# Optimization experiments

Measured on AMD Instinct MI355X. Metric: run time of the kernel, lower is better.

The kernel has to match this reference:

```python
import jax, jax.numpy as jnp
import numpy as np

N_NODES = 100000
N_EDGES = 1000000
D_IN, D_HID, D_OUT = 20, 64, 64
NEG_SLOPE = 0.2


def _gat_layer(x, src, dst, W, a_src, a_dst, b, n_nodes):
    """PyG-style single-head GATConv: message j->i, softmax over incoming edges of i."""
    h = x @ W                                  # [N, D]
    alpha_s = h @ a_src                        # [N]
    alpha_d = h @ a_dst                        # [N]
    e = jax.nn.leaky_relu(alpha_s[src] + alpha_d[dst], NEG_SLOPE)  # [E]
    # numerically-stable segment softmax over destination nodes
    m = jax.ops.segment_max(e, dst, num_segments=n_nodes)          # [N]
    ex = jnp.exp(e - m[dst])                                       # [E]
    denom = jax.ops.segment_sum(ex, dst, num_segments=n_nodes)     # [N]
    alpha = ex / denom[dst]                                        # [E]
    out = jax.ops.segment_sum(alpha[:, None] * h[src], dst, num_segments=n_nodes)
    return out + b


def setup_inputs() -> dict:
    key = jax.random.key(0)
    ks = jax.random.split(key, 11)
    x = jax.random.normal(ks[0], (N_NODES, D_IN), dtype=jnp.float32)
    edge_index = jax.random.randint(ks[1], (2, N_EDGES), 0, N_NODES, dtype=jnp.int64)
    s1 = 1.0 / np.sqrt(D_IN)
    s2 = 1.0 / np.sqrt(D_HID)
    return {
        "x": x,
        "edge_index": edge_index,
        "W1": jax.random.normal(ks[2], (D_IN, D_HID), dtype=jnp.float32) * s1,
        "a_src1": jax.random.normal(ks[3], (D_HID,), dtype=jnp.float32) * s2,
        "a_dst1": jax.random.normal(ks[4], (D_HID,), dtype=jnp.float32) * s2,
        "b1": jnp.zeros((D_HID,), dtype=jnp.float32),
        "W2": jax.random.normal(ks[5], (D_HID, D_OUT), dtype=jnp.float32) * s2,
        "a_src2": jax.random.normal(ks[6], (D_OUT,), dtype=jnp.float32) * s2,
        "a_dst2": jax.random.normal(ks[7], (D_OUT,), dtype=jnp.float32) * s2,
        "b2": jnp.zeros((D_OUT,), dtype=jnp.float32),
    }


def reference(x, edge_index, W1, a_src1, a_dst1, b1, W2, a_src2, a_dst2, b2):
    n = x.shape[0]
    # PyG GATConv adds self-loops by default
    loops = jnp.arange(n, dtype=edge_index.dtype)
    src = jnp.concatenate([edge_index[0], loops])
    dst = jnp.concatenate([edge_index[1], loops])
    h = _gat_layer(x, src, dst, W1, a_src1, a_dst1, b1, n)
    h = jax.nn.relu(h)
    # dropout(p=0.2) is identity in eval mode
    h = _gat_layer(h, src, dst, W2, a_src2, a_dst2, b2, n)
    # global_mean_pool with all-zero batch -> mean over all nodes, shape [1, D_OUT]
    return jnp.mean(h, axis=0, keepdims=True)
```

## Files before the change

### kernel.cpp

```cpp
#include <hip/hip_runtime.h>
#include <math.h>

#define NDIM 64
#define LRELU_SLOPE 0.2f
#define BSHIFT 8
#define BNODES 256
#define ECAP 3584
#define CCAP (ECAP + BNODES)

typedef float f32x2 __attribute__((ext_vector_type(2)));

__device__ __forceinline__ ushort f2bf(float f) {
    unsigned u = __float_as_uint(f);
    unsigned r = (u + 0x7fffu + ((u >> 16) & 1u)) >> 16;
    return (ushort)r;
}
__device__ __forceinline__ float bflo(unsigned u) { return __uint_as_float(u << 16); }
__device__ __forceinline__ float bfhi(unsigned u) { return __uint_as_float(u & 0xffff0000u); }

__global__ __launch_bounds__(256) void pg_kernel(
    const int* __restrict__ src, const int* __restrict__ dst,
    int* __restrict__ bcur, unsigned* __restrict__ part, int E, int nb, int PB,
    const float* __restrict__ X, const float* __restrict__ W,
    const float* __restrict__ asrc, const float* __restrict__ adst,
    unsigned char* __restrict__ h, float* __restrict__ as_,
    float* __restrict__ ad_, int N) {
    int t = threadIdx.x;
    if ((int)blockIdx.x < PB) {
        __shared__ int hist[512];
        __shared__ int base[512];
        for (int i = t; i < nb; i += 256) hist[i] = 0;
        __syncthreads();
        int chunk = blockIdx.x * 2048;
        int s[8], d[8];
#pragma unroll
        for (int j = 0; j < 2; ++j) {
            int idx = chunk + j * 1024 + t * 4;
            if (idx + 3 < E) {
                int4 sv = *(const int4*)(src + idx);
                int4 dv = *(const int4*)(dst + idx);
                s[j*4+0]=sv.x; s[j*4+1]=sv.y; s[j*4+2]=sv.z; s[j*4+3]=sv.w;
                d[j*4+0]=dv.x; d[j*4+1]=dv.y; d[j*4+2]=dv.z; d[j*4+3]=dv.w;
            } else {
#pragma unroll
                for (int q = 0; q < 4; ++q) {
                    int i2 = idx + q;
                    if (i2 < E) { s[j*4+q] = src[i2]; d[j*4+q] = dst[i2]; }
                    else        { s[j*4+q] = 0;       d[j*4+q] = -1; }
                }
            }
        }
#pragma unroll
        for (int j = 0; j < 8; ++j)
            if (d[j] >= 0) atomicAdd(&hist[d[j] >> BSHIFT], 1);
        __syncthreads();
        for (int i = t; i < nb; i += 256) {
            int c = hist[i];
            base[i] = c ? atomicAdd(&bcur[i], c) : 0;
            hist[i] = 0;
        }
        __syncthreads();
#pragma unroll
        for (int j = 0; j < 8; ++j) {
            if (d[j] >= 0) {
                int b = d[j] >> BSHIFT;
                int loc = base[b] + atomicAdd(&hist[b], 1);
                if (loc > ECAP - 1) loc = ECAP - 1;
                part[(size_t)b * ECAP + loc] =
                    ((unsigned)(d[j] & (BNODES - 1)) << 17) | (unsigned)s[j];
            }
        }
    } else {
        const int K = 20, KS = 32;
        __shared__ float xs[64 * 32];
        __shared__ unsigned hsq[64 * 17];
        __shared__ float ps[2][4][64];
        int base2 = (blockIdx.x - PB) * 64;
        for (int i = t; i < 64 * KS; i += 256) {
            int nl = i / KS, k = i - nl * KS;
            int node = base2 + nl;
            float v = (k < K && node < N) ? X[(size_t)node * K + k] : 0.f;
            xs[nl * KS + ((k + nl) & (KS - 1))] = v;
        }
        __syncthreads();
        int wid = __builtin_amdgcn_readfirstlane(t >> 6);
        int lane = t & 63;
        int node = base2 + lane;
        float acc[16];
#pragma unroll
        for (int j = 0; j < 16; ++j) acc[j] = 0.f;
        const float* Wg = W + wid * 16;
        const float* xrow = xs + lane * KS;
#pragma unroll 4
        for (int k = 0; k < K; ++k) {
            float xk = xrow[(k + lane) & (KS - 1)];
#pragma unroll
            for (int j = 0; j < 16; ++j)
                acc[j] = fmaf(xk, Wg[k * 64 + j], acc[j]);
        }
        float s = 0.f, d = 0.f;
#pragma unroll
        for (int j = 0; j < 16; ++j) {
            s = fmaf(acc[j], asrc[wid * 16 + j], s);
            d = fmaf(acc[j], adst[wid * 16 + j], d);
        }
        ps[0][wid][lane] = s;
        ps[1][wid][lane] = d;
#pragma unroll
        for (int j = 0; j < 16; j += 4) {
            int q = (wid * 16 + j) >> 2;
            int sp = (q + lane) & 15;
            int u = __builtin_amdgcn_cvt_pk_fp8_f32(acc[j], acc[j + 1], 0, false);
            u = __builtin_amdgcn_cvt_pk_fp8_f32(acc[j + 2], acc[j + 3], u, true);
            hsq[lane * 17 + sp] = (unsigned)u;
        }
        __syncthreads();
        if (wid == 0) {
            float s4 = ps[0][0][lane] + ps[0][1][lane] + ps[0][2][lane] + ps[0][3][lane];
            float d4 = ps[1][0][lane] + ps[1][1][lane] + ps[1][2][lane] + ps[1][3][lane];
            if (node < N) { as_[node] = s4; ad_[node] = d4; }
        }
        unsigned* hout = (unsigned*)h;
        for (int pass = 0; pass < 4; ++pass) {
            int row = pass * 16 + (t >> 4);
            int q = t & 15;
            int sp = (q + row) & 15;
            unsigned v = hsq[row * 17 + sp];
            int n2 = base2 + row;
            if (n2 < N) hout[(size_t)n2 * 16 + q] = v;
        }
    }
}

__global__ __launch_bounds__(256) void csr_kernel(
    const int* __restrict__ bcur, const unsigned* __restrict__ part,
    int* __restrict__ csr, int2* __restrict__ offlen, int N,
    const float* __restrict__ W2, const float* __restrict__ a_src2,
    const float* __restrict__ a_dst2, float* __restrict__ atil) {
    __shared__ int hist[256];
    __shared__ int sc[256];
    int b = blockIdx.x, t = threadIdx.x;
    int nodeBase = b << BSHIFT;
    int nNodes = min(BNODES, N - nodeBase);
    int count = min(bcur[b], ECAP);
    hist[t] = (t < nNodes) ? 1 : 0;
    __syncthreads();
    const unsigned* slice = part + (size_t)b * ECAP;
    for (int i = t; i < count; i += 256) {
        int dl = (int)(slice[i] >> 17);
        atomicAdd(&hist[dl], 1);
    }
    __syncthreads();
    int cnt = hist[t];
    sc[t] = cnt;
    __syncthreads();
    for (int o = 1; o < 256; o <<= 1) {
        int v = sc[t];
        int u = (t >= o) ? sc[t - o] : 0;
        __syncthreads();
        sc[t] = v + u;
        __syncthreads();
    }
    int excl = sc[t] - cnt;
    int boff = b * CCAP;
    if (t < nNodes) {
        offlen[nodeBase + t] = make_int2(boff + excl, cnt);
        csr[boff + excl] = nodeBase + t;
    }
    hist[t] = excl + 1;
    __syncthreads();
    for (int i = t; i < count; i += 256) {
        unsigned e = slice[i];
        int dl = (int)(e >> 17);
        int pos = boff + atomicAdd(&hist[dl], 1);
        csr[pos] = (int)(e & 0x1ffffu);
    }
    if (b == 0 && t < 128) {
        int j = t & 63;
        const float* av = (t < 64) ? a_src2 : a_dst2;
        const float* wr = W2 + (size_t)j * 64;
        float s = 0.f;
#pragma unroll 8
        for (int k = 0; k < 64; ++k) s = fmaf(wr[k], av[k], s);
        atil[t] = s;
    }
}

__global__ __launch_bounds__(256) void agg1_kernel(
    const int2* __restrict__ offlen, const int* __restrict__ csr,
    const float* __restrict__ as_, const float* __restrict__ ad_,
    const unsigned char* __restrict__ hsrc, const float* __restrict__ bias,
    const float* __restrict__ atil,
    ushort* __restrict__ out, float* __restrict__ as2,
    float* __restrict__ ad2, int n) {
    int wid = threadIdx.x >> 6, lane = threadIdx.x & 63;
    int half = lane >> 5;
    int lh = lane & 31;
    int g = lh >> 3;
    int l = lane & 7;
    int hw = wid * 2 + half;
    int node = blockIdx.x * 8 + hw;
    int base_lane = lane & 32;
    if (node < n) {
        int2 ol = offlen[node];
        int off = ol.x, len = ol.y;
        float adi = ad_[node];
        bool vpre = lh < len;
        int skpre = vpre ? csr[off + lh] : 0;
        float apre = vpre ? as_[skpre] : 0.f;
        float tpre = apre + adi;
        tpre = (tpre > 0.f) ? tpre : LRELU_SLOPE * tpre;
        float expre = vpre ? __expf(tpre) : 0.f;
        float den = expre;
        den += __shfl_xor(den, 1);
        den += __shfl_xor(den, 2);
        den += __shfl_xor(den, 4);
        den += __shfl_xor(den, 8);
        den += __shfl_xor(den, 16);
        float acc[8];
#pragma unroll
        for (int j = 0; j < 8; ++j) acc[j] = 0.f;
        if (__all(len <= 32)) {
            uint2 hv[8];
            float exs[8];
#pragma unroll
            for (int c = 0; c < 8; ++c) {
                int e = c * 4 + g;
                int sk = __shfl(skpre, base_lane + e);
                exs[c] = __shfl(expre, base_lane + e);
                const uint2* p = (const uint2*)(hsrc + ((size_t)sk << 6) + (l << 3));
                hv[c] = (e < len) ? *p : make_uint2(0u, 0u);
            }
#pragma unroll
            for (int c = 0; c < 8; ++c) {
                float ex = exs[c];
                f32x2 p0 = __builtin_amdgcn_cvt_pk_f32_fp8(hv[c].x, false);
                f32x2 p1 = __builtin_amdgcn_cvt_pk_f32_fp8(hv[c].x, true);
                f32x2 p2 = __builtin_amdgcn_cvt_pk_f32_fp8(hv[c].y, false);
                f32x2 p3 = __builtin_amdgcn_cvt_pk_f32_fp8(hv[c].y, true);
                acc[0] = fmaf(ex, p0.x, acc[0]);
                acc[1] = fmaf(ex, p0.y, acc[1]);
                acc[2] = fmaf(ex, p1.x, acc[2]);
                acc[3] = fmaf(ex, p1.y, acc[3]);
                acc[4] = fmaf(ex, p2.x, acc[4]);
                acc[5] = fmaf(ex, p2.y, acc[5]);
                acc[6] = fmaf(ex, p3.x, acc[6]);
                acc[7] = fmaf(ex, p3.y, acc[7]);
            }
        } else {
            float den_tail = 0.f;
            int niter = (len + 3) >> 2;
            int sk0 = __shfl(skpre, base_lane + g);
            float ex0 = __shfl(expre, base_lane + g);
            bool ve0 = g < len;
            uint2 hv0 = make_uint2(0, 0);
            if (ve0) hv0 = *(const uint2*)(hsrc + ((size_t)sk0 << 6) + (l << 3));
            int sk1 = __shfl(skpre, base_lane + 4 + g);
            float ex1 = __shfl(expre, base_lane + 4 + g);
            bool ve1 = (4 + g) < len;
            uint2 hv1 = make_uint2(0, 0);
            if (ve1) hv1 = *(const uint2*)(hsrc + ((size_t)sk1 << 6) + (l << 3));
            for (int i = 0; i < niter; ++i) {
                float ex = ex0;
                uint2 hv = hv0;
                ex0 = ex1; hv0 = hv1;
                int e2 = (i + 2) * 4 + g;
                bool ve2 = e2 < len;
                int esrc = e2 < 32 ? e2 : 31;
                sk1 = __shfl(skpre, base_lane + esrc);
                ex1 = __shfl(expre, base_lane + esrc);
                if (e2 >= 32) {
                    if (ve2) {
                        sk1 = csr[off + e2];
                        float a = as_[sk1];
                        float tt = a + adi;
                        tt = (tt > 0.f) ? tt : LRELU_SLOPE * tt;
                        ex1 = __expf(tt);
                        den_tail += ex1;
                    } else ex1 = 0.f;
                }
                hv1 = make_uint2(0, 0);
                if (ve2) hv1 = *(const uint2*)(hsrc + ((size_t)sk1 << 6) + (l << 3));
                f32x2 p0 = __builtin_amdgcn_cvt_pk_f32_fp8(hv.x, false);
                f32x2 p1 = __builtin_amdgcn_cvt_pk_f32_fp8(hv.x, true);
                f32x2 p2 = __builtin_amdgcn_cvt_pk_f32_fp8(hv.y, false);
                f32x2 p3 = __builtin_amdgcn_cvt_pk_f32_fp8(hv.y, true);
                acc[0] = fmaf(ex, p0.x, acc[0]);
                acc[1] = fmaf(ex, p0.y, acc[1]);
                acc[2] = fmaf(ex, p1.x, acc[2]);
                acc[3] = fmaf(ex, p1.y, acc[3]);
                acc[4] = fmaf(ex, p2.x, acc[4]);
                acc[5] = fmaf(ex, p2.y, acc[5]);
                acc[6] = fmaf(ex, p3.x, acc[6]);
                acc[7] = fmaf(ex, p3.y, acc[7]);
            }
            den_tail += __shfl_xor(den_tail, 8);
            den_tail += __shfl_xor(den_tail, 16);
            den += den_tail;
        }
#pragma unroll
        for (int j = 0; j < 8; ++j) {
            acc[j] += __shfl_xor(acc[j], 8);
            acc[j] += __shfl_xor(acc[j], 16);
        }
        float inv = 1.f / den;
        const float4 bv0 = *(const float4*)(bias + l * 8);
        const float4 bv1 = *(const float4*)(bias + l * 8 + 4);
        float v[8];
        v[0] = fmaxf(fmaf(acc[0], inv, bv0.x), 0.f);
        v[1] = fmaxf(fmaf(acc[1], inv, bv0.y), 0.f);
        v[2] = fmaxf(fmaf(acc[2], inv, bv0.z), 0.f);
        v[3] = fmaxf(fmaf(acc[3], inv, bv0.w), 0.f);
        v[4] = fmaxf(fmaf(acc[4], inv, bv1.x), 0.f);
        v[5] = fmaxf(fmaf(acc[5], inv, bv1.y), 0.f);
        v[6] = fmaxf(fmaf(acc[6], inv, bv1.z), 0.f);
        v[7] = fmaxf(fmaf(acc[7], inv, bv1.w), 0.f);
        if (g == 0) {
            uint4 pk;
            pk.x = (unsigned)f2bf(v[0]) | ((unsigned)f2bf(v[1]) << 16);
            pk.y = (unsigned)f2bf(v[2]) | ((unsigned)f2bf(v[3]) << 16);
            pk.z = (unsigned)f2bf(v[4]) | ((unsigned)f2bf(v[5]) << 16);
            pk.w = (unsigned)f2bf(v[6]) | ((unsigned)f2bf(v[7]) << 16);
            *(uint4*)(out + (size_t)node * NDIM + l * 8) = pk;
        }
        const float4 s0 = *(const float4*)(atil + l * 8);
        const float4 s1 = *(const float4*)(atil + l * 8 + 4);
        const float4 d0 = *(const float4*)(atil + 64 + l * 8);
        const float4 d1 = *(const float4*)(atil + 64 + l * 8 + 4);
        float sp = v[0]*s0.x + v[1]*s0.y + v[2]*s0.z + v[3]*s0.w
                 + v[4]*s1.x + v[5]*s1.y + v[6]*s1.z + v[7]*s1.w;
        float dp = v[0]*d0.x + v[1]*d0.y + v[2]*d0.z + v[3]*d0.w
                 + v[4]*d1.x + v[5]*d1.y + v[6]*d1.z + v[7]*d1.w;
        sp += __shfl_xor(sp, 1); sp += __shfl_xor(sp, 2); sp += __shfl_xor(sp, 4);
        dp += __shfl_xor(dp, 1); dp += __shfl_xor(dp, 2); dp += __shfl_xor(dp, 4);
        if (lh == 0) { as2[node] = sp; ad2[node] = dp; }
    }
}

__global__ __launch_bounds__(256) void agg2_kernel(
    const int2* __restrict__ offlen, const int* __restrict__ csr,
    const float* __restrict__ as_, const float* __restrict__ ad_,
    const ushort* __restrict__ osrc, float* __restrict__ pool, int n) {
    __shared__ float psum[8][NDIM];
    int wid = threadIdx.x >> 6, lane = threadIdx.x & 63;
    int half = lane >> 5;
    int lh = lane & 31;
    int g = lh >> 3;
    int l = lane & 7;
    int hw = wid * 2 + half;
    int node = blockIdx.x * 8 + hw;
    int base_lane = lane & 32;
    float v[8];
#pragma unroll
    for (int j = 0; j < 8; ++j) v[j] = 0.f;
    if (node < n) {
        int2 ol = offlen[node];
        int off = ol.x, len = ol.y;
        float adi = ad_[node];
        bool vpre = lh < len;
        int skpre = vpre ? csr[off + lh] : 0;
        float apre = vpre ? as_[skpre] : 0.f;
        float tpre = apre + adi;
        tpre = (tpre > 0.f) ? tpre : LRELU_SLOPE * tpre;
        float expre = vpre ? __expf(tpre) : 0.f;
        float den = expre;
        den += __shfl_xor(den, 1);
        den += __shfl_xor(den, 2);
        den += __shfl_xor(den, 4);
        den += __shfl_xor(den, 8);
        den += __shfl_xor(den, 16);
        float acc[8];
#pragma unroll
        for (int j = 0; j < 8; ++j) acc[j] = 0.f;
        if (__all(len <= 32)) {
            uint4 hv[8];
            float exs[8];
#pragma unroll
            for (int c = 0; c < 8; ++c) {
                int e = c * 4 + g;
                int sk = __shfl(skpre, base_lane + e);
                exs[c] = __shfl(expre, base_lane + e);
                const uint4* p = (const uint4*)(osrc + ((size_t)sk << 6) + (l << 3));
                hv[c] = (e < len) ? *p : make_uint4(0u, 0u, 0u, 0u);
            }
#pragma unroll
            for (int c = 0; c < 8; ++c) {
                float ex = exs[c];
                acc[0] = fmaf(ex, bflo(hv[c].x), acc[0]);
                acc[1] = fmaf(ex, bfhi(hv[c].x), acc[1]);
                acc[2] = fmaf(ex, bflo(hv[c].y), acc[2]);
                acc[3] = fmaf(ex, bfhi(hv[c].y), acc[3]);
                acc[4] = fmaf(ex, bflo(hv[c].z), acc[4]);
                acc[5] = fmaf(ex, bfhi(hv[c].z), acc[5]);
                acc[6] = fmaf(ex, bflo(hv[c].w), acc[6]);
                acc[7] = fmaf(ex, bfhi(hv[c].w), acc[7]);
            }
        } else {
            float den_tail = 0.f;
            int niter = (len + 3) >> 2;
            int sk0 = __shfl(skpre, base_lane + g);
            float ex0 = __shfl(expre, base_lane + g);
            bool ve0 = g < len;
            uint4 hv0 = make_uint4(0, 0, 0, 0);
            if (ve0) hv0 = *(const uint4*)(osrc + ((size_t)sk0 << 6) + (l << 3));
            int sk1 = __shfl(skpre, base_lane + 4 + g);
            float ex1 = __shfl(expre, base_lane + 4 + g);
            bool ve1 = (4 + g) < len;
            uint4 hv1 = make_uint4(0, 0, 0, 0);
            if (ve1) hv1 = *(const uint4*)(osrc + ((size_t)sk1 << 6) + (l << 3));
            for (int i = 0; i < niter; ++i) {
                float ex = ex0;
                uint4 hv = hv0;
                ex0 = ex1; hv0 = hv1;
                int e2 = (i + 2) * 4 + g;
                bool ve2 = e2 < len;
                int esrc = e2 < 32 ? e2 : 31;
                sk1 = __shfl(skpre, base_lane + esrc);
                ex1 = __shfl(expre, base_lane + esrc);
                if (e2 >= 32) {
                    if (ve2) {
                        sk1 = csr[off + e2];
                        float a = as_[sk1];
                        float tt = a + adi;
                        tt = (tt > 0.f) ? tt : LRELU_SLOPE * tt;
                        ex1 = __expf(tt);
                        den_tail += ex1;
                    } else ex1 = 0.f;
                }
                hv1 = make_uint4(0, 0, 0, 0);
                if (ve2) hv1 = *(const uint4*)(osrc + ((size_t)sk1 << 6) + (l << 3));
                acc[0] = fmaf(ex, bflo(hv.x), acc[0]);
                acc[1] = fmaf(ex, bfhi(hv.x), acc[1]);
                acc[2] = fmaf(ex, bflo(hv.y), acc[2]);
                acc[3] = fmaf(ex, bfhi(hv.y), acc[3]);
                acc[4] = fmaf(ex, bflo(hv.z), acc[4]);
                acc[5] = fmaf(ex, bfhi(hv.z), acc[5]);
                acc[6] = fmaf(ex, bflo(hv.w), acc[6]);
                acc[7] = fmaf(ex, bfhi(hv.w), acc[7]);
            }
            den_tail += __shfl_xor(den_tail, 8);
            den_tail += __shfl_xor(den_tail, 16);
            den += den_tail;
        }
#pragma unroll
        for (int j = 0; j < 8; ++j) {
            acc[j] += __shfl_xor(acc[j], 8);
            acc[j] += __shfl_xor(acc[j], 16);
        }
        float inv = 1.f / den;
#pragma unroll
        for (int j = 0; j < 8; ++j) v[j] = acc[j] * inv;
    }
    if (g == 0) {
#pragma unroll
        for (int j = 0; j < 8; ++j) psum[hw][l * 8 + j] = v[j];
    }
    __syncthreads();
    if (threadIdx.x < NDIM) {
        float t = 0.f;
#pragma unroll
        for (int r = 0; r < 8; ++r) t += psum[r][threadIdx.x];
        pool[(size_t)blockIdx.x * NDIM + threadIdx.x] = t;
    }
}

__global__ void mean_kernel(const float* __restrict__ pool,
                            const float* __restrict__ W2,
                            const float* __restrict__ b2,
                            float* __restrict__ out, int nb, float invn) {
    __shared__ float sm[4][NDIM];
    __shared__ float zs[NDIM];
    int lane = threadIdx.x & 63, wid = threadIdx.x >> 6;
    int row = blockIdx.x * 4 + wid;
    int stride = gridDim.x * 4;
    float s = 0.f;
    for (int i = row; i < nb; i += stride) s += pool[(long)i * NDIM + lane];
    sm[wid][lane] = s;
    __syncthreads();
    if (wid == 0) {
        zs[lane] = sm[0][lane] + sm[1][lane] + sm[2][lane] + sm[3][lane];
    }
    __syncthreads();
    if (wid == 0) {
        float y = 0.f;
#pragma unroll 8
        for (int j = 0; j < 64; ++j)
            y = fmaf(zs[j], W2[(size_t)j * 64 + lane], y);
        atomicAdd(&out[lane], y * invn);
        if (blockIdx.x == 0) atomicAdd(&out[lane], b2[lane]);
    }
}

extern "C" void kernel_launch(void* const* d_in, const int* in_sizes, int n_in,
                              void* d_out, int out_size, void* d_ws, size_t ws_size,
                              hipStream_t stream) {
    const float* x      = (const float*)d_in[0];
    const int*   eidx   = (const int*)d_in[1];
    const float* W1     = (const float*)d_in[2];
    const float* a_src1 = (const float*)d_in[3];
    const float* a_dst1 = (const float*)d_in[4];
    const float* b1     = (const float*)d_in[5];
    const float* W2     = (const float*)d_in[6];
    const float* a_src2 = (const float*)d_in[7];
    const float* a_dst2 = (const float*)d_in[8];
    const float* b2     = (const float*)d_in[9];
    float* out = (float*)d_out;

    const int N = in_sizes[0] / 20;
    const int E = in_sizes[1] / 2;
    const int* src = eidx;
    const int* dst = eidx + E;
    const int NB = (N + BNODES - 1) >> BSHIFT;

    const int gemm_blocks = (N + 63) / 64;
    const int agg_blocks  = (N + 7) / 8;
    const int PB = (E + 2047) / 2048;

    char* ws = (char*)d_ws;
    unsigned char* h = (unsigned char*)ws;
    ushort* o   = (ushort*)(h + (size_t)N * NDIM);
    float* as1  = (float*)(o + (size_t)N * NDIM);
    float* ad1  = as1 + N;
    float* as2  = ad1 + N;
    float* ad2  = as2 + N;
    int2*  offlen = (int2*)(ad2 + N);
    int*   csr  = (int*)(offlen + N);
    float* pool = (float*)(csr + (size_t)NB * CCAP);
    float* atil = pool + (size_t)agg_blocks * NDIM;
    int*   bcur = (int*)(atil + 128);
    unsigned* part = (unsigned*)(bcur + NB);

    hipMemsetAsync(d_out, 0, (size_t)out_size * sizeof(float), stream);
    hipMemsetAsync(bcur, 0, (size_t)NB * sizeof(int), stream);

    pg_kernel<<<PB + gemm_blocks, 256, 0, stream>>>(
        src, dst, bcur, part, E, NB, PB,
        x, W1, a_src1, a_dst1, h, as1, ad1, N);
    csr_kernel<<<NB, 256, 0, stream>>>(bcur, part, csr, offlen, N,
                                       W2, a_src2, a_dst2, atil);

    agg1_kernel<<<agg_blocks, 256, 0, stream>>>(
        offlen, csr, as1, ad1, h, b1, atil, o, as2, ad2, N);

    agg2_kernel<<<agg_blocks, 256, 0, stream>>>(
        offlen, csr, as2, ad2, o, pool, N);

    mean_kernel<<<64, 256, 0, stream>>>(pool, W2, b2, out, agg_blocks,
                                        1.0f / (float)N);
}
```

Before: 193.8 us.

## Store layer-1 output as FP8 and share a packed-math gather helper

The layer-1 aggregated activations are now stored as FP8 instead of bf16, which halves the bytes gathered per edge in the second aggregation kernel. Both aggregation kernels now call a common gather routine that accumulates with packed two-wide f32 multiply-adds and skips chunks that are fully past the longest row in the wave pair. Out-of-range nodes are clamped rather than branched around. The cost is lower precision in the intermediate activations, which may move the result further from the reference.

```diff
diff --git a/kernel.cpp b/kernel.cpp
--- a/kernel.cpp
+++ b/kernel.cpp
@@ -10,11 +10,6 @@
 
 typedef float f32x2 __attribute__((ext_vector_type(2)));
 
-__device__ __forceinline__ ushort f2bf(float f) {
-    unsigned u = __float_as_uint(f);
-    unsigned r = (u + 0x7fffu + ((u >> 16) & 1u)) >> 16;
-    return (ushort)r;
-}
 __device__ __forceinline__ float bflo(unsigned u) { return __uint_as_float(u << 16); }
 __device__ __forceinline__ float bfhi(unsigned u) { return __uint_as_float(u & 0xffff0000u); }
 
@@ -186,12 +181,110 @@
     }
 }
 
+__device__ __forceinline__ float gather64(
+    int off, int len, int lm, float adi, int lh, int g, int l, int base_lane,
+    const int* __restrict__ csr, const float* __restrict__ as_,
+    const unsigned char* __restrict__ rows, float acc[8]) {
+    bool vpre = lh < len;
+    int skpre = vpre ? csr[off + lh] : 0;
+    float apre = vpre ? as_[skpre] : 0.f;
+    float tpre = apre + adi;
+    tpre = (tpre > 0.f) ? tpre : LRELU_SLOPE * tpre;
+    float expre = vpre ? __expf(tpre) : 0.f;
+    float den = expre;
+    den += __shfl_xor(den, 1);
+    den += __shfl_xor(den, 2);
+    den += __shfl_xor(den, 4);
+    den += __shfl_xor(den, 8);
+    den += __shfl_xor(den, 16);
+    f32x2 a01 = {0.f, 0.f}, a23 = {0.f, 0.f}, a45 = {0.f, 0.f}, a67 = {0.f, 0.f};
+    if (__all(lm <= 32)) {
+        uint2 hv[8];
+        float exs[8];
+#pragma unroll
+        for (int c = 0; c < 8; ++c) {
+            hv[c] = make_uint2(0u, 0u);
+            exs[c] = 0.f;
+            if (c * 4 < lm) {
+                int e = c * 4 + g;
+                int sk = __shfl(skpre, base_lane + e);
+                exs[c] = __shfl(expre, base_lane + e);
+                if (e < len)
+                    hv[c] = *(const uint2*)(rows + ((size_t)sk << 6) + (l << 3));
+            }
+        }
+#pragma unroll
+        for (int c = 0; c < 8; ++c) {
+            if (c * 4 < len) {
+                f32x2 ex2 = {exs[c], exs[c]};
+                a01 += __builtin_amdgcn_cvt_pk_f32_fp8(hv[c].x, false) * ex2;
+                a23 += __builtin_amdgcn_cvt_pk_f32_fp8(hv[c].x, true) * ex2;
+                a45 += __builtin_amdgcn_cvt_pk_f32_fp8(hv[c].y, false) * ex2;
+                a67 += __builtin_amdgcn_cvt_pk_f32_fp8(hv[c].y, true) * ex2;
+            }
+        }
+    } else {
+        float den_tail = 0.f;
+        int niter = (len + 3) >> 2;
+        int sk0 = __shfl(skpre, base_lane + g);
+        float ex0 = __shfl(expre, base_lane + g);
+        bool ve0 = g < len;
+        uint2 hv0 = make_uint2(0, 0);
+        if (ve0) hv0 = *(const uint2*)(rows + ((size_t)sk0 << 6) + (l << 3));
+        int sk1 = __shfl(skpre, base_lane + 4 + g);
+        float ex1 = __shfl(expre, base_lane + 4 + g);
+        bool ve1 = (4 + g) < len;
+        uint2 hv1 = make_uint2(0, 0);
+        if (ve1) hv1 = *(const uint2*)(rows + ((size_t)sk1 << 6) + (l << 3));
+        for (int i = 0; i < niter; ++i) {
+            float ex = ex0;
+            uint2 hv = hv0;
+            ex0 = ex1; hv0 = hv1;
+            int e2 = (i + 2) * 4 + g;
+            bool ve2 = e2 < len;
+            int esrc = e2 < 32 ? e2 : 31;
+            sk1 = __shfl(skpre, base_lane + esrc);
+            ex1 = __shfl(expre, base_lane + esrc);
+            if (e2 >= 32) {
+                if (ve2) {
+                    sk1 = csr[off + e2];
+                    float a = as_[sk1];
+                    float tt = a + adi;
+                    tt = (tt > 0.f) ? tt : LRELU_SLOPE * tt;
+                    ex1 = __expf(tt);
+                    den_tail += ex1;
+                } else ex1 = 0.f;
+            }
+            hv1 = make_uint2(0, 0);
+            if (ve2) hv1 = *(const uint2*)(rows + ((size_t)sk1 << 6) + (l << 3));
+            f32x2 ex2 = {ex, ex};
+            a01 += __builtin_amdgcn_cvt_pk_f32_fp8(hv.x, false) * ex2;
+            a23 += __builtin_amdgcn_cvt_pk_f32_fp8(hv.x, true) * ex2;
+            a45 += __builtin_amdgcn_cvt_pk_f32_fp8(hv.y, false) * ex2;
+            a67 += __builtin_amdgcn_cvt_pk_f32_fp8(hv.y, true) * ex2;
+        }
+        den_tail += __shfl_xor(den_tail, 8);
+        den_tail += __shfl_xor(den_tail, 16);
+        den += den_tail;
+    }
+    acc[0] = a01.x; acc[1] = a01.y;
+    acc[2] = a23.x; acc[3] = a23.y;
+    acc[4] = a45.x; acc[5] = a45.y;
+    acc[6] = a67.x; acc[7] = a67.y;
+#pragma unroll
+    for (int j = 0; j < 8; ++j) {
+        acc[j] += __shfl_xor(acc[j], 8);
+        acc[j] += __shfl_xor(acc[j], 16);
+    }
+    return den;
+}
+
 __global__ __launch_bounds__(256) void agg1_kernel(
     const int2* __restrict__ offlen, const int* __restrict__ csr,
     const float* __restrict__ as_, const float* __restrict__ ad_,
     const unsigned char* __restrict__ hsrc, const float* __restrict__ bias,
     const float* __restrict__ atil,
-    ushort* __restrict__ out, float* __restrict__ as2,
+    unsigned char* __restrict__ o8, float* __restrict__ as2,
     float* __restrict__ ad2, int n) {
     int wid = threadIdx.x >> 6, lane = threadIdx.x & 63;
     int half = lane >> 5;
@@ -201,108 +294,16 @@
     int hw = wid * 2 + half;
     int node = blockIdx.x * 8 + hw;
     int base_lane = lane & 32;
+    int nodec = min(node, n - 1);
+    int2 ol = offlen[nodec];
+    int off = ol.x;
+    int len = (node < n) ? ol.y : 0;
+    float adi = ad_[nodec];
+    int lm = max(len, __shfl_xor(len, 32));
+    float acc[8];
+    float den = gather64(off, len, lm, adi, lh, g, l, base_lane,
+                         csr, as_, hsrc, acc);
     if (node < n) {
-        int2 ol = offlen[node];
-        int off = ol.x, len = ol.y;
-        float adi = ad_[node];
-        bool vpre = lh < len;
-        int skpre = vpre ? csr[off + lh] : 0;
-        float apre = vpre ? as_[skpre] : 0.f;
-        float tpre = apre + adi;
-        tpre = (tpre > 0.f) ? tpre : LRELU_SLOPE * tpre;
-        float expre = vpre ? __expf(tpre) : 0.f;
-        float den = expre;
-        den += __shfl_xor(den, 1);
-        den += __shfl_xor(den, 2);
-        den += __shfl_xor(den, 4);
-        den += __shfl_xor(den, 8);
-        den += __shfl_xor(den, 16);
-        float acc[8];
-#pragma unroll
-        for (int j = 0; j < 8; ++j) acc[j] = 0.f;
-        if (__all(len <= 32)) {
-            uint2 hv[8];
-            float exs[8];
-#pragma unroll
-            for (int c = 0; c < 8; ++c) {
-                int e = c * 4 + g;
-                int sk = __shfl(skpre, base_lane + e);
-                exs[c] = __shfl(expre, base_lane + e);
-                const uint2* p = (const uint2*)(hsrc + ((size_t)sk << 6) + (l << 3));
-                hv[c] = (e < len) ? *p : make_uint2(0u, 0u);
-            }
-#pragma unroll
-            for (int c = 0; c < 8; ++c) {
-                float ex = exs[c];
-                f32x2 p0 = __builtin_amdgcn_cvt_pk_f32_fp8(hv[c].x, false);
-                f32x2 p1 = __builtin_amdgcn_cvt_pk_f32_fp8(hv[c].x, true);
-                f32x2 p2 = __builtin_amdgcn_cvt_pk_f32_fp8(hv[c].y, false);
-                f32x2 p3 = __builtin_amdgcn_cvt_pk_f32_fp8(hv[c].y, true);
-                acc[0] = fmaf(ex, p0.x, acc[0]);
-                acc[1] = fmaf(ex, p0.y, acc[1]);
-                acc[2] = fmaf(ex, p1.x, acc[2]);
-                acc[3] = fmaf(ex, p1.y, acc[3]);
-                acc[4] = fmaf(ex, p2.x, acc[4]);
-                acc[5] = fmaf(ex, p2.y, acc[5]);
-                acc[6] = fmaf(ex, p3.x, acc[6]);
-                acc[7] = fmaf(ex, p3.y, acc[7]);
-            }
-        } else {
-            float den_tail = 0.f;
-            int niter = (len + 3) >> 2;
-            int sk0 = __shfl(skpre, base_lane + g);
-            float ex0 = __shfl(expre, base_lane + g);
-            bool ve0 = g < len;
-            uint2 hv0 = make_uint2(0, 0);
-            if (ve0) hv0 = *(const uint2*)(hsrc + ((size_t)sk0 << 6) + (l << 3));
-            int sk1 = __shfl(skpre, base_lane + 4 + g);
-            float ex1 = __shfl(expre, base_lane + 4 + g);
-            bool ve1 = (4 + g) < len;
-            uint2 hv1 = make_uint2(0, 0);
-            if (ve1) hv1 = *(const uint2*)(hsrc + ((size_t)sk1 << 6) + (l << 3));
-            for (int i = 0; i < niter; ++i) {
-                float ex = ex0;
-                uint2 hv = hv0;
-                ex0 = ex1; hv0 = hv1;
-                int e2 = (i + 2) * 4 + g;
-                bool ve2 = e2 < len;
-                int esrc = e2 < 32 ? e2 : 31;
-                sk1 = __shfl(skpre, base_lane + esrc);
-                ex1 = __shfl(expre, base_lane + esrc);
-                if (e2 >= 32) {
-                    if (ve2) {
-                        sk1 = csr[off + e2];
-                        float a = as_[sk1];
-                        float tt = a + adi;
-                        tt = (tt > 0.f) ? tt : LRELU_SLOPE * tt;
-                        ex1 = __expf(tt);
-                        den_tail += ex1;
-                    } else ex1 = 0.f;
-                }
-                hv1 = make_uint2(0, 0);
-                if (ve2) hv1 = *(const uint2*)(hsrc + ((size_t)sk1 << 6) + (l << 3));
-                f32x2 p0 = __builtin_amdgcn_cvt_pk_f32_fp8(hv.x, false);
-                f32x2 p1 = __builtin_amdgcn_cvt_pk_f32_fp8(hv.x, true);
-                f32x2 p2 = __builtin_amdgcn_cvt_pk_f32_fp8(hv.y, false);
-                f32x2 p3 = __builtin_amdgcn_cvt_pk_f32_fp8(hv.y, true);
-                acc[0] = fmaf(ex, p0.x, acc[0]);
-                acc[1] = fmaf(ex, p0.y, acc[1]);
-                acc[2] = fmaf(ex, p1.x, acc[2]);
-                acc[3] = fmaf(ex, p1.y, acc[3]);
-                acc[4] = fmaf(ex, p2.x, acc[4]);
-                acc[5] = fmaf(ex, p2.y, acc[5]);
-                acc[6] = fmaf(ex, p3.x, acc[6]);
-                acc[7] = fmaf(ex, p3.y, acc[7]);
-            }
-            den_tail += __shfl_xor(den_tail, 8);
-            den_tail += __shfl_xor(den_tail, 16);
-            den += den_tail;
-        }
-#pragma unroll
-        for (int j = 0; j < 8; ++j) {
-            acc[j] += __shfl_xor(acc[j], 8);
-            acc[j] += __shfl_xor(acc[j], 16);
-        }
         float inv = 1.f / den;
         const float4 bv0 = *(const float4*)(bias + l * 8);
         const float4 bv1 = *(const float4*)(bias + l * 8 + 4);
@@ -316,12 +317,12 @@
         v[6] = fmaxf(fmaf(acc[6], inv, bv1.z), 0.f);
         v[7] = fmaxf(fmaf(acc[7], inv, bv1.w), 0.f);
         if (g == 0) {
-            uint4 pk;
-            pk.x = (unsigned)f2bf(v[0]) | ((unsigned)f2bf(v[1]) << 16);
-            pk.y = (unsigned)f2bf(v[2]) | ((unsigned)f2bf(v[3]) << 16);
-            pk.z = (unsigned)f2bf(v[4]) | ((unsigned)f2bf(v[5]) << 16);
-            pk.w = (unsigned)f2bf(v[6]) | ((unsigned)f2bf(v[7]) << 16);
-            *(uint4*)(out + (size_t)node * NDIM + l * 8) = pk;
+            int u0 = __builtin_amdgcn_cvt_pk_fp8_f32(v[0], v[1], 0, false);
+            u0 = __builtin_amdgcn_cvt_pk_fp8_f32(v[2], v[3], u0, true);
+            int u1 = __builtin_amdgcn_cvt_pk_fp8_f32(v[4], v[5], 0, false);
+            u1 = __builtin_amdgcn_cvt_pk_fp8_f32(v[6], v[7], u1, true);
+            *(uint2*)(o8 + ((size_t)node << 6) + (l << 3)) =
+                make_uint2((unsigned)u0, (unsigned)u1);
         }
         const float4 s0 = *(const float4*)(atil + l * 8);
         const float4 s1 = *(const float4*)(atil + l * 8 + 4);
@@ -340,7 +341,7 @@
 __global__ __launch_bounds__(256) void agg2_kernel(
     const int2* __restrict__ offlen, const int* __restrict__ csr,
     const float* __restrict__ as_, const float* __restrict__ ad_,
-    const ushort* __restrict__ osrc, float* __restrict__ pool, int n) {
+    const unsigned char* __restrict__ osrc, float* __restrict__ pool, int n) {
     __shared__ float psum[8][NDIM];
     int wid = threadIdx.x >> 6, lane = threadIdx.x & 63;
     int half = lane >> 5;
@@ -350,103 +351,19 @@
     int hw = wid * 2 + half;
     int node = blockIdx.x * 8 + hw;
     int base_lane = lane & 32;
+    int nodec = min(node, n - 1);
+    int2 ol = offlen[nodec];
+    int off = ol.x;
+    int len = (node < n) ? ol.y : 0;
+    float adi = ad_[nodec];
+    int lm = max(len, __shfl_xor(len, 32));
+    float acc[8];
+    float den = gather64(off, len, lm, adi, lh, g, l, base_lane,
+                         csr, as_, osrc, acc);
     float v[8];
 #pragma unroll
     for (int j = 0; j < 8; ++j) v[j] = 0.f;
     if (node < n) {
-        int2 ol = offlen[node];
-        int off = ol.x, len = ol.y;
-        float adi = ad_[node];
-        bool vpre = lh < len;
-        int skpre = vpre ? csr[off + lh] : 0;
-        float apre = vpre ? as_[skpre] : 0.f;
-        float tpre = apre + adi;
-        tpre = (tpre > 0.f) ? tpre : LRELU_SLOPE * tpre;
-        float expre = vpre ? __expf(tpre) : 0.f;
-        float den = expre;
-        den += __shfl_xor(den, 1);
-        den += __shfl_xor(den, 2);
-        den += __shfl_xor(den, 4);
-        den += __shfl_xor(den, 8);
-        den += __shfl_xor(den, 16);
-        float acc[8];
-#pragma unroll
-        for (int j = 0; j < 8; ++j) acc[j] = 0.f;
-        if (__all(len <= 32)) {
-            uint4 hv[8];
-            float exs[8];
-#pragma unroll
-            for (int c = 0; c < 8; ++c) {
-                int e = c * 4 + g;
-                int sk = __shfl(skpre, base_lane + e);
-                exs[c] = __shfl(expre, base_lane + e);
-                const uint4* p = (const uint4*)(osrc + ((size_t)sk << 6) + (l << 3));
-                hv[c] = (e < len) ? *p : make_uint4(0u, 0u, 0u, 0u);
-            }
-#pragma unroll
-            for (int c = 0; c < 8; ++c) {
-                float ex = exs[c];
-                acc[0] = fmaf(ex, bflo(hv[c].x), acc[0]);
-                acc[1] = fmaf(ex, bfhi(hv[c].x), acc[1]);
-                acc[2] = fmaf(ex, bflo(hv[c].y), acc[2]);
-                acc[3] = fmaf(ex, bfhi(hv[c].y), acc[3]);
-                acc[4] = fmaf(ex, bflo(hv[c].z), acc[4]);
-                acc[5] = fmaf(ex, bfhi(hv[c].z), acc[5]);
-                acc[6] = fmaf(ex, bflo(hv[c].w), acc[6]);
-                acc[7] = fmaf(ex, bfhi(hv[c].w), acc[7]);
-            }
-        } else {
-            float den_tail = 0.f;
-            int niter = (len + 3) >> 2;
-            int sk0 = __shfl(skpre, base_lane + g);
-            float ex0 = __shfl(expre, base_lane + g);
-            bool ve0 = g < len;
-            uint4 hv0 = make_uint4(0, 0, 0, 0);
-            if (ve0) hv0 = *(const uint4*)(osrc + ((size_t)sk0 << 6) + (l << 3));
-            int sk1 = __shfl(skpre, base_lane + 4 + g);
-            float ex1 = __shfl(expre, base_lane + 4 + g);
-            bool ve1 = (4 + g) < len;
-            uint4 hv1 = make_uint4(0, 0, 0, 0);
-            if (ve1) hv1 = *(const uint4*)(osrc + ((size_t)sk1 << 6) + (l << 3));
-            for (int i = 0; i < niter; ++i) {
-                float ex = ex0;
-                uint4 hv = hv0;
-                ex0 = ex1; hv0 = hv1;
-                int e2 = (i + 2) * 4 + g;
-                bool ve2 = e2 < len;
-                int esrc = e2 < 32 ? e2 : 31;
-                sk1 = __shfl(skpre, base_lane + esrc);
-                ex1 = __shfl(expre, base_lane + esrc);
-                if (e2 >= 32) {
-                    if (ve2) {
-                        sk1 = csr[off + e2];
-                        float a = as_[sk1];
-                        float tt = a + adi;
-                        tt = (tt > 0.f) ? tt : LRELU_SLOPE * tt;
-                        ex1 = __expf(tt);
-                        den_tail += ex1;
-                    } else ex1 = 0.f;
-                }
-                hv1 = make_uint4(0, 0, 0, 0);
-                if (ve2) hv1 = *(const uint4*)(osrc + ((size_t)sk1 << 6) + (l << 3));
-                acc[0] = fmaf(ex, bflo(hv.x), acc[0]);
-                acc[1] = fmaf(ex, bfhi(hv.x), acc[1]);
-                acc[2] = fmaf(ex, bflo(hv.y), acc[2]);
-                acc[3] = fmaf(ex, bfhi(hv.y), acc[3]);
-                acc[4] = fmaf(ex, bflo(hv.z), acc[4]);
-                acc[5] = fmaf(ex, bfhi(hv.z), acc[5]);
-                acc[6] = fmaf(ex, bflo(hv.w), acc[6]);
-                acc[7] = fmaf(ex, bfhi(hv.w), acc[7]);
-            }
-            den_tail += __shfl_xor(den_tail, 8);
-            den_tail += __shfl_xor(den_tail, 16);
-            den += den_tail;
-        }
-#pragma unroll
-        for (int j = 0; j < 8; ++j) {
-            acc[j] += __shfl_xor(acc[j], 8);
-            acc[j] += __shfl_xor(acc[j], 16);
-        }
         float inv = 1.f / den;
 #pragma unroll
         for (int j = 0; j < 8; ++j) v[j] = acc[j] * inv;
@@ -517,9 +434,9 @@
     const int PB = (E + 2047) / 2048;
 
     char* ws = (char*)d_ws;
-    unsigned char* h = (unsigned char*)ws;
-    ushort* o   = (ushort*)(h + (size_t)N * NDIM);
-    float* as1  = (float*)(o + (size_t)N * NDIM);
+    unsigned char* h  = (unsigned char*)ws;
+    unsigned char* o8 = h + (size_t)N * NDIM;
+    float* as1  = (float*)(o8 + (size_t)N * NDIM);
     float* ad1  = as1 + N;
     float* as2  = ad1 + N;
     float* ad2  = as2 + N;
@@ -540,10 +457,10 @@
                                        W2, a_src2, a_dst2, atil);
 
     agg1_kernel<<<agg_blocks, 256, 0, stream>>>(
-        offlen, csr, as1, ad1, h, b1, atil, o, as2, ad2, N);
+        offlen, csr, as1, ad1, h, b1, atil, o8, as2, ad2, N);
 
     agg2_kernel<<<agg_blocks, 256, 0, stream>>>(
-        offlen, csr, as2, ad2, o, pool, N);
+        offlen, csr, as2, ad2, o8, pool, N);
 
     mean_kernel<<<64, 256, 0, stream>>>(pool, W2, b2, out, agg_blocks,
                                         1.0f / (float)N);
```

Measured after the change: 184.7 us, median of 2. -4.7%, faster.
